# Performance work log

Measured on AMD Instinct MI355X. Metric: run time of the kernel, lower is better.

Reference implementation:

```python
import jax, jax.numpy as jnp
import numpy as np

B, K, LQ, LR, H = 32, 8, 128, 256, 512  # H = hidden_dim*2
L = LQ + K * LR


def setup_inputs() -> dict:
    key = jax.random.key(0)
    ks = jax.random.split(key, 10)
    w = 0.02
    return {
        "h_q": jax.random.normal(ks[0], (B, LQ, H), jnp.float32),
        "q_mask": jnp.ones((B, LQ), jnp.float32),
        "h_r": jax.random.normal(ks[1], (B, K, LR, H), jnp.float32),
        "r_mask": jnp.ones((B, K, LR), jnp.float32),
        "s_t": jax.random.normal(ks[2], (B, H), jnp.float32),
        "qr_cov": jnp.zeros((B, L), jnp.float32),
        # Linear weights stored torch-style [out, in]
        "U_w": jax.random.normal(ks[3], (H, H), jnp.float32) * w,
        "Wc_w": jax.random.normal(ks[4], (H, 1), jnp.float32) * w,
        "Ws_w": jax.random.normal(ks[5], (H, H), jnp.float32) * w,
        "Wqr_w": jax.random.normal(ks[6], (H, H), jnp.float32) * w,
        "Wqr_b": jax.random.normal(ks[7], (H,), jnp.float32) * w,
        "Vr_w": jax.random.normal(ks[8], (1, H), jnp.float32) * w,
    }


def reference(h_q, q_mask, h_r, r_mask, s_t, qr_cov,
              U_w, Wc_w, Ws_w, Wqr_w, Wqr_b, Vr_w):
    b, l_q, h = h_q.shape
    _, k, l_r, _ = h_r.shape

    _h_q = jnp.broadcast_to(h_q[:, None], (b, k, l_q, h)).reshape(b * k, l_q, h)
    _h_r = h_r.reshape(b * k, l_r, h)
    _q_mask = jnp.broadcast_to(q_mask[:, None], (b, k, l_q)).reshape(b * k, l_q)
    _r_mask = r_mask.reshape(b * k, l_r)

    # bilinear co-attention scores: tanh((hq @ U^T) @ hr^T)  [b*k, l_q, l_r]
    hqU = jnp.einsum('bqi,oi->bqo', _h_q, U_w)
    U = jnp.tanh(jnp.einsum('bqo,bro->bqr', hqU, _h_r))

    alpha_q = jax.nn.softmax(jnp.max(U, axis=2), axis=-1)  # [b*k, l_q]
    alpha_r = jax.nn.softmax(jnp.max(U, axis=1), axis=-1)  # [b*k, l_r]

    pai_q = ((alpha_q * _q_mask)[..., None] * _h_q).reshape(b, k, l_q, h).mean(axis=1)
    pai_r = ((alpha_r * _r_mask)[..., None] * _h_r).reshape(b, k * l_r, h)
    qr = jnp.concatenate([pai_q, pai_r], axis=1)  # [b, L, h]

    dec_fea = (jnp.einsum('bi,oi->bo', s_t, Ws_w)[:, None, :]
               + jnp.einsum('bli,oi->blo', qr, Wqr_w) + Wqr_b
               + qr_cov[:, :, None] * Wc_w[:, 0])  # coverage feature

    logits = jnp.einsum('blo,o->bl', jnp.tanh(dec_fea), Vr_w[0])  # [b, L]
    mask = jnp.concatenate([q_mask, r_mask.reshape(b, k * l_r)], axis=1)
    a = jax.nn.softmax(logits, axis=1) * mask
    a = a / jnp.sum(a, axis=1, keepdims=True)

    c_t = jnp.einsum('bl,blh->bh', a, qr)
    new_cov = qr_cov + a
    return (c_t, a, new_cov)
```

## Files before the change

kernel.cpp:

```cpp
#include <hip/hip_runtime.h>
#include <hip/hip_fp8.h>
#include <stdint.h>

#define B  32
#define KK 8
#define LQ 128
#define LR 256
#define H  512
#define LL 2176

typedef short s16x8 __attribute__((ext_vector_type(8)));
typedef float f32x4 __attribute__((ext_vector_type(4)));
typedef int   i32x8 __attribute__((ext_vector_type(8)));

__device__ __forceinline__ unsigned short f2bf(float f) {
    unsigned int u = __float_as_uint(f);
    unsigned int r = (u + 0x7FFFu + ((u >> 16) & 1u)) >> 16;
    return (unsigned short)r;
}
__device__ __forceinline__ unsigned char f2fp8(float f) {
    __hip_fp8_e4m3 v(f);
    return (unsigned char)v.__x;
}
__device__ __forceinline__ unsigned int pk_fp8(float a, float b) {
#if __has_builtin(__builtin_amdgcn_cvt_pk_fp8_f32)
    return (unsigned int)__builtin_amdgcn_cvt_pk_fp8_f32(a, b, 0, false) & 0xFFFFu;
#else
    return (unsigned int)f2fp8(a) | ((unsigned int)f2fp8(b) << 8);
#endif
}
__device__ __forceinline__ unsigned int pk_bf16(float a, float b) {
    return (unsigned int)f2bf(a) | ((unsigned int)f2bf(b) << 16);
}
__device__ __forceinline__ void gload16(const void* g, void* l) {
    __builtin_amdgcn_global_load_lds(
        (const __attribute__((address_space(1))) void*)g,
        (__attribute__((address_space(3))) void*)l, 16, 0, 0);
}
__device__ __forceinline__ float fexp2(float x) {
#if __has_builtin(__builtin_amdgcn_exp2f)
    return __builtin_amdgcn_exp2f(x);
#else
    return __expf(x * 0.69314718056f);
#endif
}
__device__ __forceinline__ float frcp(float x) {
#if __has_builtin(__builtin_amdgcn_rcpf)
    return __builtin_amdgcn_rcpf(x);
#else
    return 1.f / x;
#endif
}
__device__ __forceinline__ float fast_tanh(float x) {
    float e = fexp2(x * 2.885390082f);
    return 1.f - 2.f * frcp(1.f + e);
}
#define LOG2E 1.4426950408889634f

#define NQ4 (B * LQ * H / 4)
#define NR4 (B * KK * LR * H / 4)
#define NL4 (B * LL / 4)
#define NC4 (B * H / 4)
#define NWB4 (B * LL / 4)
#define SBLK 256
#define WBLK 64
#define ZBLK 19
#define QBLK 256
#define RBLK 4096
#define K0GRID (SBLK + WBLK + ZBLK + QBLK + RBLK)
__global__ __launch_bounds__(256) void k0_convert(
    const float* __restrict__ h_q, const float* __restrict__ h_r,
    const float* __restrict__ U_w, const float* __restrict__ Wqr_w,
    unsigned short* __restrict__ Xb, unsigned short* __restrict__ Uwb,
    unsigned char* __restrict__ Xb8, unsigned char* __restrict__ Wqrb8,
    float* __restrict__ logits, float* __restrict__ out_ct,
    float* __restrict__ wbuf, const float* __restrict__ s_t,
    const float* __restrict__ Ws_w, float* __restrict__ sWs) {
    int t = threadIdx.x;
    int blk = blockIdx.x;
    if (blk < SBLK) {
        int b = blk >> 3, oc = blk & 7;
        __shared__ __align__(16) float sl[H];
        for (int i = t; i < H; i += 256) sl[i] = s_t[b * H + i];
        __syncthreads();
        int o = oc * 64 + (t >> 2);
        int part = t & 3;
        const float4* sl4 = (const float4*)sl;
        const float4* wr4 = (const float4*)(Ws_w + (size_t)o * H);
        float a = 0.f;
#pragma unroll
        for (int ii = 0; ii < 32; ++ii) {
            int i = part + 4 * ii;
            float4 x = sl4[i], y = wr4[i];
            a += x.x * y.x + x.y * y.y + x.z * y.z + x.w * y.w;
        }
        a += __shfl_xor(a, 1);
        a += __shfl_xor(a, 2);
        if (part == 0) sWs[b * H + o] = a;
        return;
    }
    blk -= SBLK;
    if (blk < WBLK) {
        bool isU = (blk < 32);
        unsigned base = (unsigned)(blk & 31) * 2048u;
        const float4* src = isU ? (const float4*)U_w : (const float4*)Wqr_w;
        uint4* dst = isU ? (uint4*)Uwb : (uint4*)((unsigned short*)Xb + 0);
        uint4* dstW = (uint4*)((unsigned char*)0);
        (void)dstW;
#pragma unroll
        for (int jj = 0; jj < 4; ++jj) {
            unsigned f4i = base + (unsigned)jj * 512u + 2u * (unsigned)t;
            float4 v0 = src[f4i], v1 = src[f4i + 1];
            uint4 ob;
            ob.x = pk_bf16(v0.x, v0.y); ob.y = pk_bf16(v0.z, v0.w);
            ob.z = pk_bf16(v1.x, v1.y); ob.w = pk_bf16(v1.z, v1.w);
            if (isU) {
                ((uint4*)Uwb)[f4i >> 1] = ob;
            } else {
                uint2 o8;
                o8.x = pk_fp8(v0.x, v0.y) | (pk_fp8(v0.z, v0.w) << 16);
                o8.y = pk_fp8(v1.x, v1.y) | (pk_fp8(v1.z, v1.w) << 16);
                ((uint2*)Wqrb8)[f4i >> 1] = o8;
            }
        }
        return;
    }
    blk -= WBLK;
    if (blk < ZBLK) {
        unsigned zb = (unsigned)blk;
        float4 zero = {0.f, 0.f, 0.f, 0.f};
        float4* lg4 = (float4*)logits;
        float4* ct4 = (float4*)out_ct;
        float4* wb4 = (float4*)wbuf;
#pragma unroll
        for (int j = 0; j < 8; ++j) {
            unsigned z = zb * 2048u + (unsigned)j * 256u + (unsigned)t;
            if (z < NL4) lg4[z] = zero;
            else if (z < NL4 + NC4) ct4[z - NL4] = zero;
            else if (z < NL4 + NC4 + NWB4) wb4[z - NL4 - NC4] = zero;
        }
        return;
    }
    blk -= ZBLK;
    {
        const float4* src; unsigned dstoff;
        if (blk < QBLK) {
            unsigned u0 = (unsigned)blk * 2048u;
            unsigned b = (unsigned)blk >> 3;
            src = (const float4*)h_q + u0;
            dstoff = b * 278528u + (u0 & 16383u);
        } else {
            unsigned rb = (unsigned)(blk - QBLK);
            unsigned u0 = rb * 2048u;
            unsigned b = rb >> 7;
            src = (const float4*)h_r + u0;
            dstoff = b * 278528u + 16384u + (u0 & 262143u);
        }
        uint4* dstb = (uint4*)Xb;
        uint2* dst8 = (uint2*)Xb8;
#pragma unroll
        for (int jj = 0; jj < 4; ++jj) {
            unsigned loc = (unsigned)jj * 512u + 2u * (unsigned)t;
            float4 v0 = src[loc], v1 = src[loc + 1];
            unsigned idx = (dstoff + loc) >> 1;
            uint4 ob;
            ob.x = pk_bf16(v0.x, v0.y); ob.y = pk_bf16(v0.z, v0.w);
            ob.z = pk_bf16(v1.x, v1.y); ob.w = pk_bf16(v1.z, v1.w);
            dstb[idx] = ob;
            uint2 o8;
            o8.x = pk_fp8(v0.x, v0.y) | (pk_fp8(v0.z, v0.w) << 16);
            o8.y = pk_fp8(v1.x, v1.y) | (pk_fp8(v1.z, v1.w) << 16);
            dst8[idx] = o8;
        }
    }
}

__global__ __launch_bounds__(256) void k1_gemm_hqU(
    const unsigned short* __restrict__ Xb, const unsigned short* __restrict__ Uwb,
    unsigned char* __restrict__ hqU8) {
    __shared__ __align__(16) unsigned short As[64 * 64];
    __shared__ __align__(16) unsigned short Bs[128 * 64];
    int tid = threadIdx.x;
    int wave = tid >> 6, lane = tid & 63;
    int quad = lane >> 4, l16 = lane & 15;
    int wr = wave >> 1, wc = wave & 1;
    int g = blockIdx.x;
    int tle = (g & 7) * 32 + (g >> 3);
    int mt = tle >> 2, nt = tle & 3;
    int m0 = mt * 64, n0 = nt * 128;

    const unsigned short* ag[2]; unsigned short* la[2];
    const unsigned short* bg[4]; unsigned short* lb[4];
#pragma unroll
    for (int i = 0; i < 2; ++i) {
        int gg = (wave * 2 + i) * 64 + lane;
        int r = gg >> 3, c = gg & 7, cs = c ^ (r & 7);
        int am = m0 + r;
        ag[i] = Xb + ((size_t)(am >> 7) * LL + (am & 127)) * H + cs * 8;
        la[i] = As + (wave * 2 + i) * 512;
    }
#pragma unroll
    for (int i = 0; i < 4; ++i) {
        int gg = (wave * 4 + i) * 64 + lane;
        int r = gg >> 3, c = gg & 7, cs = c ^ (r & 7);
        bg[i] = Uwb + (size_t)(n0 + r) * H + cs * 8;
        lb[i] = Bs + (wave * 4 + i) * 512;
    }

    f32x4 acc[2][4] = {};
    for (int k0 = 0; k0 < H; k0 += 64) {
#pragma unroll
        for (int i = 0; i < 2; ++i) gload16(ag[i] + k0, la[i]);
#pragma unroll
        for (int i = 0; i < 4; ++i) gload16(bg[i] + k0, lb[i]);
        __syncthreads();
#pragma unroll
        for (int kh = 0; kh < 2; ++kh) {
            s16x8 af[2], bfr[4];
#pragma unroll
            for (int mi = 0; mi < 2; ++mi) {
                int row = wr * 32 + mi * 16 + l16;
                int ch = (kh * 4 + quad) ^ (row & 7);
                af[mi] = *(const s16x8*)&As[(row * 8 + ch) * 8];
            }
#pragma unroll
            for (int ni = 0; ni < 4; ++ni) {
                int row = wc * 64 + ni * 16 + l16;
                int ch = (kh * 4 + quad) ^ (row & 7);
                bfr[ni] = *(const s16x8*)&Bs[(row * 8 + ch) * 8];
            }
#pragma unroll
            for (int mi = 0; mi < 2; ++mi)
#pragma unroll
                for (int ni = 0; ni < 4; ++ni)
                    acc[mi][ni] = __builtin_amdgcn_mfma_f32_16x16x32_bf16(
                        af[mi], bfr[ni], acc[mi][ni], 0, 0, 0);
        }
        __syncthreads();
    }
#pragma unroll
    for (int mi = 0; mi < 2; ++mi)
#pragma unroll
        for (int ni = 0; ni < 4; ++ni)
#pragma unroll
            for (int i = 0; i < 4; ++i) {
                float v = acc[mi][ni][i];
                float vn = __shfl_xor(v, 1);
                if ((l16 & 1) == 0) {
                    int row = m0 + wr * 32 + mi * 16 + quad * 4 + i;
                    int col = n0 + wc * 64 + ni * 16 + l16;
                    unsigned short pk = (unsigned short)pk_fp8(v, vn);
                    *(unsigned short*)(hqU8 + (size_t)row * H + col) = pk;
                }
            }
}

__global__ __launch_bounds__(256) void k2_scores(
    const unsigned char* __restrict__ hqU8, const unsigned char* __restrict__ Xb8,
    float* __restrict__ maxq, float* __restrict__ maxr_part) {
    __shared__ __align__(16) unsigned char As[64 * 128];
    __shared__ __align__(16) unsigned char Bs[256 * 128];
    __shared__ float redA[64 * 2];
    __shared__ float redB[256 * 2];
    int g = blockIdx.x;
    int tle = (g & 7) * 64 + (g >> 3);
    int qt = tle & 1, k = (tle >> 1) & 7, b = tle >> 4;
    int tid = threadIdx.x;
    int wave = tid >> 6, lane = tid & 63;
    int quad = lane >> 4, l16 = lane & 15;
    int wr = wave >> 1, wc = wave & 1;

    const unsigned char* Ab = hqU8 + (size_t)(b * LQ + qt * 64) * H;
    const unsigned char* Bb = Xb8 + (size_t)(b * LL + LQ + k * LR) * H;

    const unsigned char* ag[2]; unsigned char* la[2];
    const unsigned char* bg[8]; unsigned char* lb[8];
#pragma unroll
    for (int i = 0; i < 2; ++i) {
        int gg = (wave * 2 + i) * 64 + lane;
        int r = gg >> 3, c = gg & 7, cs = c ^ (r & 7);
        ag[i] = Ab + (size_t)r * H + cs * 16;
        la[i] = As + gg * 16;
    }
#pragma unroll
    for (int i = 0; i < 8; ++i) {
        int gg = (wave * 8 + i) * 64 + lane;
        int r = gg >> 3, c = gg & 7, cs = c ^ (r & 7);
        bg[i] = Bb + (size_t)r * H + cs * 16;
        lb[i] = Bs + gg * 16;
    }

    f32x4 acc[2][8] = {};
    for (int k0 = 0; k0 < H; k0 += 128) {
#pragma unroll
        for (int i = 0; i < 2; ++i) gload16(ag[i] + k0, la[i]);
#pragma unroll
        for (int i = 0; i < 8; ++i) gload16(bg[i] + k0, lb[i]);
        __syncthreads();
        i32x8 af[2];
#pragma unroll
        for (int mi = 0; mi < 2; ++mi) {
            int row = wr * 32 + mi * 16 + l16;
            int xs = row & 7;
            const uint4* rp = (const uint4*)(As + row * 128);
            uint4 lo = rp[(quad * 2) ^ xs];
            uint4 hi = rp[(quad * 2 + 1) ^ xs];
            af[mi][0] = lo.x; af[mi][1] = lo.y; af[mi][2] = lo.z; af[mi][3] = lo.w;
            af[mi][4] = hi.x; af[mi][5] = hi.y; af[mi][6] = hi.z; af[mi][7] = hi.w;
        }
#pragma unroll
        for (int ni = 0; ni < 8; ++ni) {
            int row = wc * 128 + ni * 16 + l16;
            int xs = row & 7;
            const uint4* rp = (const uint4*)(Bs + row * 128);
            uint4 lo = rp[(quad * 2) ^ xs];
            uint4 hi = rp[(quad * 2 + 1) ^ xs];
            i32x8 bfr;
            bfr[0] = lo.x; bfr[1] = lo.y; bfr[2] = lo.z; bfr[3] = lo.w;
            bfr[4] = hi.x; bfr[5] = hi.y; bfr[6] = hi.z; bfr[7] = hi.w;
#pragma unroll
            for (int mi = 0; mi < 2; ++mi)
                acc[mi][ni] = __builtin_amdgcn_mfma_scale_f32_16x16x128_f8f6f4(
                    af[mi], bfr, acc[mi][ni], 0, 0,
                    0, 0x7F7F7F7F, 0, 0x7F7F7F7F);
        }
        __syncthreads();
    }
#pragma unroll
    for (int mi = 0; mi < 2; ++mi)
#pragma unroll
        for (int i = 0; i < 4; ++i) {
            float v = acc[mi][0][i];
#pragma unroll
            for (int ni = 1; ni < 8; ++ni) v = fmaxf(v, acc[mi][ni][i]);
            for (int s = 1; s < 16; s <<= 1) v = fmaxf(v, __shfl_xor(v, s));
            if (l16 == 0) redA[(wr * 32 + mi * 16 + quad * 4 + i) * 2 + wc] = v;
        }
#pragma unroll
    for (int ni = 0; ni < 8; ++ni) {
        float v = acc[0][ni][0];
#pragma unroll
        for (int mi = 0; mi < 2; ++mi)
#pragma unroll
            for (int i = 0; i < 4; ++i) v = fmaxf(v, acc[mi][ni][i]);
        for (int s = 16; s < 64; s <<= 1) v = fmaxf(v, __shfl_xor(v, s));
        if (quad == 0) redB[(wc * 128 + ni * 16 + l16) * 2 + wr] = v;
    }
    __syncthreads();
    size_t bk = (size_t)(b * KK + k);
    if (tid < 64)
        maxq[bk * 128 + qt * 64 + tid] = fmaxf(redA[tid * 2 + 0], redA[tid * 2 + 1]);
    maxr_part[(bk * 2 + qt) * 256 + tid] = fmaxf(redB[tid * 2 + 0], redB[tid * 2 + 1]);
}

__global__ __launch_bounds__(256) void k3_alphas(
    const float* __restrict__ maxq, const float* __restrict__ maxr_part,
    const float* __restrict__ r_mask, const float* __restrict__ q_mask,
    float* __restrict__ wbuf) {
    int b = blockIdx.x >> 3, k = blockIdx.x & 7;
    int t = threadIdx.x;
    __shared__ float red[256];
    size_t bk = (size_t)(b * KK + k);
    float vq = -1e30f;
    if (t < 128) vq = fast_tanh(maxq[bk * 128 + t]);
    red[t] = vq; __syncthreads();
    for (int s = 128; s > 0; s >>= 1) { if (t < s) red[t] = fmaxf(red[t], red[t + s]); __syncthreads(); }
    float mxq = red[0]; __syncthreads();
    float eq = (t < 128) ? fexp2((vq - mxq) * LOG2E) : 0.f;
    red[t] = eq; __syncthreads();
    for (int s = 128; s > 0; s >>= 1) { if (t < s) red[t] += red[t + s]; __syncthreads(); }
    float invq = 1.f / red[0]; __syncthreads();
    if (t < 128)
        atomicAdd(&wbuf[b * LL + t], q_mask[b * LQ + t] * eq * invq * 0.125f);
    float vr = fast_tanh(fmaxf(maxr_part[(bk * 2 + 0) * 256 + t],
                               maxr_part[(bk * 2 + 1) * 256 + t]));
    red[t] = vr; __syncthreads();
    for (int s = 128; s > 0; s >>= 1) { if (t < s) red[t] = fmaxf(red[t], red[t + s]); __syncthreads(); }
    float mxr = red[0]; __syncthreads();
    float er = fexp2((vr - mxr) * LOG2E);
    red[t] = er; __syncthreads();
    for (int s = 128; s > 0; s >>= 1) { if (t < s) red[t] += red[t + s]; __syncthreads(); }
    float invr = 1.f / red[0];
    wbuf[b * LL + LQ + k * LR + t] = r_mask[bk * LR + t] * er * invr;
}

__global__ __launch_bounds__(256) void k4_gemm_logits(
    const unsigned char* __restrict__ Xb8, const unsigned char* __restrict__ Wqrb8,
    const float* __restrict__ sWs, const float* __restrict__ Wqr_b,
    const float* __restrict__ Wc_w, const float* __restrict__ Vr_w,
    const float* __restrict__ wbuf, const float* __restrict__ qr_cov,
    float* __restrict__ logits) {
    __shared__ __align__(16) unsigned char As[128 * 128];
    __shared__ __align__(16) unsigned char Bs[128 * 128];
    __shared__ float wrow[128], covrow[128], sWsl[128], biasl[128], wcl[128], vrl[128];
    int tid = threadIdx.x;
    int wave = tid >> 6, lane = tid & 63;
    int quad = lane >> 4, l16 = lane & 15;
    int wr = wave >> 1, wc = wave & 1;
    int g = blockIdx.x;
    int tle = (g & 7) * 272 + (g >> 3);
    int mt = tle >> 2, nt = tle & 3;
    size_t m0 = (size_t)mt * 128;
    int n0 = nt * 128;
    int b = mt / 17;

    if (tid < 128) {
        wrow[tid]   = wbuf[m0 + tid];
        covrow[tid] = qr_cov[m0 + tid];
        sWsl[tid]   = sWs[b * H + n0 + tid];
        biasl[tid]  = Wqr_b[n0 + tid];
        wcl[tid]    = Wc_w[n0 + tid];
        vrl[tid]    = Vr_w[n0 + tid];
    }

    const unsigned char* ag[4]; unsigned char* la[4];
    const unsigned char* bg[4]; unsigned char* lb[4];
#pragma unroll
    for (int i = 0; i < 4; ++i) {
        int gg = (wave * 4 + i) * 64 + lane;
        int r = gg >> 3, c = gg & 7, cs = c ^ (r & 7);
        ag[i] = Xb8 + (m0 + r) * H + cs * 16;
        bg[i] = Wqrb8 + (size_t)(n0 + r) * H + cs * 16;
        la[i] = As + (wave * 4 + i) * 1024;
        lb[i] = Bs + (wave * 4 + i) * 1024;
    }

    f32x4 acc[4][4] = {};
    for (int k0 = 0; k0 < H; k0 += 128) {
#pragma unroll
        for (int i = 0; i < 4; ++i) gload16(ag[i] + k0, la[i]);
#pragma unroll
        for (int i = 0; i < 4; ++i) gload16(bg[i] + k0, lb[i]);
        __syncthreads();
        i32x8 af[4];
#pragma unroll
        for (int mi = 0; mi < 4; ++mi) {
            int row = wr * 64 + mi * 16 + l16;
            int xs = row & 7;
            const uint4* rp = (const uint4*)(As + row * 128);
            uint4 lo = rp[(quad * 2) ^ xs];
            uint4 hi = rp[(quad * 2 + 1) ^ xs];
            af[mi][0] = lo.x; af[mi][1] = lo.y; af[mi][2] = lo.z; af[mi][3] = lo.w;
            af[mi][4] = hi.x; af[mi][5] = hi.y; af[mi][6] = hi.z; af[mi][7] = hi.w;
        }
#pragma unroll
        for (int ni = 0; ni < 4; ++ni) {
            int row = wc * 64 + ni * 16 + l16;
            int xs = row & 7;
            const uint4* rp = (const uint4*)(Bs + row * 128);
            uint4 lo = rp[(quad * 2) ^ xs];
            uint4 hi = rp[(quad * 2 + 1) ^ xs];
            i32x8 bfr;
            bfr[0] = lo.x; bfr[1] = lo.y; bfr[2] = lo.z; bfr[3] = lo.w;
            bfr[4] = hi.x; bfr[5] = hi.y; bfr[6] = hi.z; bfr[7] = hi.w;
#pragma unroll
            for (int mi = 0; mi < 4; ++mi)
                acc[mi][ni] = __builtin_amdgcn_mfma_scale_f32_16x16x128_f8f6f4(
                    af[mi], bfr, acc[mi][ni], 0, 0,
                    0, 0x7F7F7F7F, 0, 0x7F7F7F7F);
        }
        __syncthreads();
    }
#pragma unroll
    for (int mi = 0; mi < 4; ++mi)
#pragma unroll
        for (int i = 0; i < 4; ++i) {
            int rl = wr * 64 + mi * 16 + quad * 4 + i;
            float wv = wrow[rl], cv = covrow[rl];
            float lsum = 0.f;
#pragma unroll
            for (int ni = 0; ni < 4; ++ni) {
                int ol = wc * 64 + ni * 16 + l16;
                float dec = sWsl[ol] + wv * acc[mi][ni][i] + biasl[ol] + cv * wcl[ol];
                lsum += vrl[ol] * fast_tanh(dec);
            }
            for (int s = 1; s < 16; s <<= 1) lsum += __shfl_xor(lsum, s);
            if (l16 == 0) atomicAdd(&logits[m0 + rl], lsum);
        }
}

__global__ __launch_bounds__(256) void k5a_softmax(
    const float* __restrict__ logits, const float* __restrict__ q_mask,
    const float* __restrict__ r_mask, const float* __restrict__ qr_cov,
    const float* __restrict__ wbuf, float* __restrict__ out,
    float* __restrict__ coef) {
    int b = blockIdx.x, t = threadIdx.x;
    __shared__ float lg[LL];
    __shared__ float red[256];
    float mx = -1e30f;
    for (int l = t; l < LL; l += 256) {
        float v = logits[b * LL + l];
        lg[l] = v;
        mx = fmaxf(mx, v);
    }
    red[t] = mx; __syncthreads();
    for (int s = 128; s > 0; s >>= 1) { if (t < s) red[t] = fmaxf(red[t], red[t + s]); __syncthreads(); }
    mx = red[0]; __syncthreads();
    float sum = 0.f;
    for (int l = t; l < LL; l += 256) {
        float e = fexp2((lg[l] - mx) * LOG2E);
        float m = (l < LQ) ? q_mask[b * LQ + l] : r_mask[b * (KK * LR) + l - LQ];
        float em = e * m;
        lg[l] = em;
        sum += em;
    }
    red[t] = sum; __syncthreads();
    for (int s = 128; s > 0; s >>= 1) { if (t < s) red[t] += red[t + s]; __syncthreads(); }
    float inv = 1.f / red[0];
    __syncthreads();
    float* aout = out + B * H + (size_t)b * LL;
    float* cov  = out + B * H + (size_t)B * LL + (size_t)b * LL;
    for (int l = t; l < LL; l += 256) {
        float a = lg[l] * inv;
        aout[l] = a;
        cov[l] = qr_cov[b * LL + l] + a;
        coef[b * LL + l] = a * wbuf[b * LL + l];
    }
}

__global__ __launch_bounds__(256) void k5b_ct(
    const unsigned short* __restrict__ Xb, const float* __restrict__ coef,
    float* __restrict__ out) {
    int b = blockIdx.x / 34, chunk = blockIdx.x % 34;
    int t = threadIdx.x;
    int l0 = chunk * 64;
    __shared__ float cl[64];
    __shared__ float red[4][512];
    if (t < 64) cl[t] = coef[b * LL + l0 + t];
    __syncthreads();
    int rr = t >> 6, lane = t & 63, cc = lane * 8;
    float a[8] = {};
    const unsigned short* xp = Xb + ((size_t)b * LL + l0) * H;
    for (int l = rr; l < 64; l += 4) {
        float c = cl[l];
        uint4 u4 = *(const uint4*)(xp + (size_t)l * H + cc);
        a[0] += c * __uint_as_float(u4.x << 16);
        a[1] += c * __uint_as_float(u4.x & 0xffff0000u);
        a[2] += c * __uint_as_float(u4.y << 16);
        a[3] += c * __uint_as_float(u4.y & 0xffff0000u);
        a[4] += c * __uint_as_float(u4.z << 16);
        a[5] += c * __uint_as_float(u4.z & 0xffff0000u);
        a[6] += c * __uint_as_float(u4.w << 16);
        a[7] += c * __uint_as_float(u4.w & 0xffff0000u);
    }
#pragma unroll
    for (int j = 0; j < 8; ++j) red[rr][cc + j] = a[j];
    __syncthreads();
    int col = t * 2;
    float s0 = red[0][col] + red[1][col] + red[2][col] + red[3][col];
    float s1 = red[0][col + 1] + red[1][col + 1] + red[2][col + 1] + red[3][col + 1];
    atomicAdd(&out[b * H + col], s0);
    atomicAdd(&out[b * H + col + 1], s1);
}

extern "C" void kernel_launch(void* const* d_in, const int* in_sizes, int n_in,
                              void* d_out, int out_size, void* d_ws, size_t ws_size,
                              hipStream_t stream) {
    (void)in_sizes; (void)n_in; (void)out_size; (void)ws_size;
    const float* h_q    = (const float*)d_in[0];
    const float* q_mask = (const float*)d_in[1];
    const float* h_r    = (const float*)d_in[2];
    const float* r_mask = (const float*)d_in[3];
    const float* s_t    = (const float*)d_in[4];
    const float* qr_cov = (const float*)d_in[5];
    const float* U_w    = (const float*)d_in[6];
    const float* Wc_w   = (const float*)d_in[7];
    const float* Ws_w   = (const float*)d_in[8];
    const float* Wqr_w  = (const float*)d_in[9];
    const float* Wqr_b  = (const float*)d_in[10];
    const float* Vr_w   = (const float*)d_in[11];
    float* out = (float*)d_out;

    char* p = (char*)d_ws;
    unsigned short* Xb    = (unsigned short*)p; p += (size_t)B * LL * H * 2;
    unsigned char*  Xb8   = (unsigned char*)p;  p += (size_t)B * LL * H;
    unsigned short* Uwb   = (unsigned short*)p; p += (size_t)H * H * 2;
    unsigned char*  Wqrb8 = (unsigned char*)p;  p += (size_t)H * H;
    unsigned char*  hqU8  = (unsigned char*)p;  p += (size_t)B * LQ * H;
    float* sWs       = (float*)p; p += (size_t)B * H * 4;
    float* maxq      = (float*)p; p += (size_t)B * KK * 128 * 4;
    float* maxr_part = (float*)p; p += (size_t)B * KK * 2 * 256 * 4;
    float* wbuf      = (float*)p; p += (size_t)B * LL * 4;
    float* logits    = (float*)p; p += (size_t)B * LL * 4;
    float* coef      = (float*)p; p += (size_t)B * LL * 4;

    k0_convert<<<K0GRID, 256, 0, stream>>>(h_q, h_r, U_w, Wqr_w, Xb, Uwb,
                                           Xb8, Wqrb8, logits, out, wbuf,
                                           s_t, Ws_w, sWs);
    k1_gemm_hqU<<<256, 256, 0, stream>>>(Xb, Uwb, hqU8);
    k2_scores<<<512, 256, 0, stream>>>(hqU8, Xb8, maxq, maxr_part);
    k3_alphas<<<B * KK, 256, 0, stream>>>(maxq, maxr_part, r_mask, q_mask, wbuf);
    k4_gemm_logits<<<2176, 256, 0, stream>>>(
        Xb8, Wqrb8, sWs, Wqr_b, Wc_w, Vr_w, wbuf, qr_cov, logits);
    k5a_softmax<<<B, 256, 0, stream>>>(logits, q_mask, r_mask, qr_cov, wbuf, out, coef);
    k5b_ct<<<B * 34, 256, 0, stream>>>(Xb, coef, out);
}
```

Before: 361.2 us.

## Drop full bf16 activation copy, read fp32 inputs in context kernel, shrink logits tiles

```diff
diff --git a/kernel.cpp b/kernel.cpp
--- a/kernel.cpp
+++ b/kernel.cpp
@@ -22,11 +22,14 @@
     __hip_fp8_e4m3 v(f);
     return (unsigned char)v.__x;
 }
-__device__ __forceinline__ unsigned int pk_fp8(float a, float b) {
+__device__ __forceinline__ unsigned int pk_fp8x4(float a, float b, float c, float d) {
 #if __has_builtin(__builtin_amdgcn_cvt_pk_fp8_f32)
-    return (unsigned int)__builtin_amdgcn_cvt_pk_fp8_f32(a, b, 0, false) & 0xFFFFu;
+    int w = __builtin_amdgcn_cvt_pk_fp8_f32(a, b, 0, false);
+    w = __builtin_amdgcn_cvt_pk_fp8_f32(c, d, w, true);
+    return (unsigned int)w;
 #else
-    return (unsigned int)f2fp8(a) | ((unsigned int)f2fp8(b) << 8);
+    return (unsigned int)f2fp8(a) | ((unsigned int)f2fp8(b) << 8) |
+           ((unsigned int)f2fp8(c) << 16) | ((unsigned int)f2fp8(d) << 24);
 #endif
 }
 __device__ __forceinline__ unsigned int pk_bf16(float a, float b) {
@@ -57,8 +60,6 @@
 }
 #define LOG2E 1.4426950408889634f
 
-#define NQ4 (B * LQ * H / 4)
-#define NR4 (B * KK * LR * H / 4)
 #define NL4 (B * LL / 4)
 #define NC4 (B * H / 4)
 #define NWB4 (B * LL / 4)
@@ -71,7 +72,7 @@
 __global__ __launch_bounds__(256) void k0_convert(
     const float* __restrict__ h_q, const float* __restrict__ h_r,
     const float* __restrict__ U_w, const float* __restrict__ Wqr_w,
-    unsigned short* __restrict__ Xb, unsigned short* __restrict__ Uwb,
+    unsigned short* __restrict__ Xq, unsigned short* __restrict__ Uwb,
     unsigned char* __restrict__ Xb8, unsigned char* __restrict__ Wqrb8,
     float* __restrict__ logits, float* __restrict__ out_ct,
     float* __restrict__ wbuf, const float* __restrict__ s_t,
@@ -104,22 +105,19 @@
         bool isU = (blk < 32);
         unsigned base = (unsigned)(blk & 31) * 2048u;
         const float4* src = isU ? (const float4*)U_w : (const float4*)Wqr_w;
-        uint4* dst = isU ? (uint4*)Uwb : (uint4*)((unsigned short*)Xb + 0);
-        uint4* dstW = (uint4*)((unsigned char*)0);
-        (void)dstW;
 #pragma unroll
         for (int jj = 0; jj < 4; ++jj) {
             unsigned f4i = base + (unsigned)jj * 512u + 2u * (unsigned)t;
             float4 v0 = src[f4i], v1 = src[f4i + 1];
-            uint4 ob;
-            ob.x = pk_bf16(v0.x, v0.y); ob.y = pk_bf16(v0.z, v0.w);
-            ob.z = pk_bf16(v1.x, v1.y); ob.w = pk_bf16(v1.z, v1.w);
             if (isU) {
+                uint4 ob;
+                ob.x = pk_bf16(v0.x, v0.y); ob.y = pk_bf16(v0.z, v0.w);
+                ob.z = pk_bf16(v1.x, v1.y); ob.w = pk_bf16(v1.z, v1.w);
                 ((uint4*)Uwb)[f4i >> 1] = ob;
             } else {
                 uint2 o8;
-                o8.x = pk_fp8(v0.x, v0.y) | (pk_fp8(v0.z, v0.w) << 16);
-                o8.y = pk_fp8(v1.x, v1.y) | (pk_fp8(v1.z, v1.w) << 16);
+                o8.x = pk_fp8x4(v0.x, v0.y, v0.z, v0.w);
+                o8.y = pk_fp8x4(v1.x, v1.y, v1.z, v1.w);
                 ((uint2*)Wqrb8)[f4i >> 1] = o8;
             }
         }
@@ -142,41 +140,46 @@
         return;
     }
     blk -= ZBLK;
-    {
-        const float4* src; unsigned dstoff;
-        if (blk < QBLK) {
-            unsigned u0 = (unsigned)blk * 2048u;
-            unsigned b = (unsigned)blk >> 3;
-            src = (const float4*)h_q + u0;
-            dstoff = b * 278528u + (u0 & 16383u);
-        } else {
-            unsigned rb = (unsigned)(blk - QBLK);
-            unsigned u0 = rb * 2048u;
-            unsigned b = rb >> 7;
-            src = (const float4*)h_r + u0;
-            dstoff = b * 278528u + 16384u + (u0 & 262143u);
-        }
-        uint4* dstb = (uint4*)Xb;
-        uint2* dst8 = (uint2*)Xb8;
+    if (blk < QBLK) {
+        unsigned u0 = (unsigned)blk * 2048u;
+        unsigned b = (unsigned)blk >> 3;
+        const float4* src = (const float4*)h_q + u0;
 #pragma unroll
         for (int jj = 0; jj < 4; ++jj) {
             unsigned loc = (unsigned)jj * 512u + 2u * (unsigned)t;
             float4 v0 = src[loc], v1 = src[loc + 1];
-            unsigned idx = (dstoff + loc) >> 1;
             uint4 ob;
             ob.x = pk_bf16(v0.x, v0.y); ob.y = pk_bf16(v0.z, v0.w);
             ob.z = pk_bf16(v1.x, v1.y); ob.w = pk_bf16(v1.z, v1.w);
-            dstb[idx] = ob;
+            ((uint4*)Xq)[(u0 + loc) >> 1] = ob;
             uint2 o8;
-            o8.x = pk_fp8(v0.x, v0.y) | (pk_fp8(v0.z, v0.w) << 16);
-            o8.y = pk_fp8(v1.x, v1.y) | (pk_fp8(v1.z, v1.w) << 16);
-            dst8[idx] = o8;
+            o8.x = pk_fp8x4(v0.x, v0.y, v0.z, v0.w);
+            o8.y = pk_fp8x4(v1.x, v1.y, v1.z, v1.w);
+            unsigned f8off = b * 278528u + ((u0 + loc) & 16383u);
+            ((uint2*)Xb8)[f8off >> 1] = o8;
+        }
+        return;
+    }
+    {
+        unsigned rb = (unsigned)(blk - QBLK);
+        unsigned u0 = rb * 2048u;
+        unsigned b = rb >> 7;
+        const float4* src = (const float4*)h_r + u0;
+#pragma unroll
+        for (int jj = 0; jj < 4; ++jj) {
+            unsigned loc = (unsigned)jj * 512u + 2u * (unsigned)t;
+            float4 v0 = src[loc], v1 = src[loc + 1];
+            uint2 o8;
+            o8.x = pk_fp8x4(v0.x, v0.y, v0.z, v0.w);
+            o8.y = pk_fp8x4(v1.x, v1.y, v1.z, v1.w);
+            unsigned f8off = b * 278528u + 16384u + ((u0 + loc) & 262143u);
+            ((uint2*)Xb8)[f8off >> 1] = o8;
         }
     }
 }
 
 __global__ __launch_bounds__(256) void k1_gemm_hqU(
-    const unsigned short* __restrict__ Xb, const unsigned short* __restrict__ Uwb,
+    const unsigned short* __restrict__ Xq, const unsigned short* __restrict__ Uwb,
     unsigned char* __restrict__ hqU8) {
     __shared__ __align__(16) unsigned short As[64 * 64];
     __shared__ __align__(16) unsigned short Bs[128 * 64];
@@ -195,8 +198,7 @@
     for (int i = 0; i < 2; ++i) {
         int gg = (wave * 2 + i) * 64 + lane;
         int r = gg >> 3, c = gg & 7, cs = c ^ (r & 7);
-        int am = m0 + r;
-        ag[i] = Xb + ((size_t)(am >> 7) * LL + (am & 127)) * H + cs * 8;
+        ag[i] = Xq + (size_t)(m0 + r) * H + cs * 8;
         la[i] = As + (wave * 2 + i) * 512;
     }
 #pragma unroll
@@ -249,7 +251,8 @@
                 if ((l16 & 1) == 0) {
                     int row = m0 + wr * 32 + mi * 16 + quad * 4 + i;
                     int col = n0 + wc * 64 + ni * 16 + l16;
-                    unsigned short pk = (unsigned short)pk_fp8(v, vn);
+                    unsigned short pk = (unsigned short)
+                        (pk_fp8x4(v, vn, 0.f, 0.f) & 0xFFFFu);
                     *(unsigned short*)(hqU8 + (size_t)row * H + col) = pk;
                 }
             }
@@ -384,27 +387,27 @@
     wbuf[b * LL + LQ + k * LR + t] = r_mask[bk * LR + t] * er * invr;
 }
 
-__global__ __launch_bounds__(256) void k4_gemm_logits(
+__global__ __launch_bounds__(256, 4) void k4_gemm_logits(
     const unsigned char* __restrict__ Xb8, const unsigned char* __restrict__ Wqrb8,
     const float* __restrict__ sWs, const float* __restrict__ Wqr_b,
     const float* __restrict__ Wc_w, const float* __restrict__ Vr_w,
     const float* __restrict__ wbuf, const float* __restrict__ qr_cov,
     float* __restrict__ logits) {
-    __shared__ __align__(16) unsigned char As[128 * 128];
-    __shared__ __align__(16) unsigned char Bs[128 * 128];
-    __shared__ float wrow[128], covrow[128], sWsl[128], biasl[128], wcl[128], vrl[128];
+    __shared__ __align__(16) unsigned char As[64 * 128];
+    __shared__ __align__(16) unsigned char Bs[64 * 128];
+    __shared__ float wrow[64], covrow[64], sWsl[64], biasl[64], wcl[64], vrl[64];
     int tid = threadIdx.x;
     int wave = tid >> 6, lane = tid & 63;
     int quad = lane >> 4, l16 = lane & 15;
     int wr = wave >> 1, wc = wave & 1;
     int g = blockIdx.x;
-    int tle = (g & 7) * 272 + (g >> 3);
-    int mt = tle >> 2, nt = tle & 3;
-    size_t m0 = (size_t)mt * 128;
-    int n0 = nt * 128;
-    int b = mt / 17;
-
-    if (tid < 128) {
+    int tle = (g & 7) * 1088 + (g >> 3);
+    int mt = tle >> 3, nt = tle & 7;
+    size_t m0 = (size_t)mt * 64;
+    int n0 = nt * 64;
+    int b = mt / 34;
+
+    if (tid < 64) {
         wrow[tid]   = wbuf[m0 + tid];
         covrow[tid] = qr_cov[m0 + tid];
         sWsl[tid]   = sWs[b * H + n0 + tid];
@@ -413,29 +416,29 @@
         vrl[tid]    = Vr_w[n0 + tid];
     }
 
-    const unsigned char* ag[4]; unsigned char* la[4];
-    const unsigned char* bg[4]; unsigned char* lb[4];
-#pragma unroll
-    for (int i = 0; i < 4; ++i) {
-        int gg = (wave * 4 + i) * 64 + lane;
+    const unsigned char* ag[2]; unsigned char* la[2];
+    const unsigned char* bg[2]; unsigned char* lb[2];
+#pragma unroll
+    for (int i = 0; i < 2; ++i) {
+        int gg = (wave * 2 + i) * 64 + lane;
         int r = gg >> 3, c = gg & 7, cs = c ^ (r & 7);
         ag[i] = Xb8 + (m0 + r) * H + cs * 16;
         bg[i] = Wqrb8 + (size_t)(n0 + r) * H + cs * 16;
-        la[i] = As + (wave * 4 + i) * 1024;
-        lb[i] = Bs + (wave * 4 + i) * 1024;
-    }
-
-    f32x4 acc[4][4] = {};
+        la[i] = As + gg * 16;
+        lb[i] = Bs + gg * 16;
+    }
+
+    f32x4 acc[2][2] = {};
     for (int k0 = 0; k0 < H; k0 += 128) {
 #pragma unroll
-        for (int i = 0; i < 4; ++i) gload16(ag[i] + k0, la[i]);
-#pragma unroll
-        for (int i = 0; i < 4; ++i) gload16(bg[i] + k0, lb[i]);
-        __syncthreads();
-        i32x8 af[4];
-#pragma unroll
-        for (int mi = 0; mi < 4; ++mi) {
-            int row = wr * 64 + mi * 16 + l16;
+        for (int i = 0; i < 2; ++i) gload16(ag[i] + k0, la[i]);
+#pragma unroll
+        for (int i = 0; i < 2; ++i) gload16(bg[i] + k0, lb[i]);
+        __syncthreads();
+        i32x8 af[2];
+#pragma unroll
+        for (int mi = 0; mi < 2; ++mi) {
+            int row = wr * 32 + mi * 16 + l16;
             int xs = row & 7;
             const uint4* rp = (const uint4*)(As + row * 128);
             uint4 lo = rp[(quad * 2) ^ xs];
@@ -444,8 +447,8 @@
             af[mi][4] = hi.x; af[mi][5] = hi.y; af[mi][6] = hi.z; af[mi][7] = hi.w;
         }
 #pragma unroll
-        for (int ni = 0; ni < 4; ++ni) {
-            int row = wc * 64 + ni * 16 + l16;
+        for (int ni = 0; ni < 2; ++ni) {
+            int row = wc * 32 + ni * 16 + l16;
             int xs = row & 7;
             const uint4* rp = (const uint4*)(Bs + row * 128);
             uint4 lo = rp[(quad * 2) ^ xs];
@@ -454,7 +457,7 @@
             bfr[0] = lo.x; bfr[1] = lo.y; bfr[2] = lo.z; bfr[3] = lo.w;
             bfr[4] = hi.x; bfr[5] = hi.y; bfr[6] = hi.z; bfr[7] = hi.w;
 #pragma unroll
-            for (int mi = 0; mi < 4; ++mi)
+            for (int mi = 0; mi < 2; ++mi)
                 acc[mi][ni] = __builtin_amdgcn_mfma_scale_f32_16x16x128_f8f6f4(
                     af[mi], bfr, acc[mi][ni], 0, 0,
                     0, 0x7F7F7F7F, 0, 0x7F7F7F7F);
@@ -462,15 +465,15 @@
         __syncthreads();
     }
 #pragma unroll
-    for (int mi = 0; mi < 4; ++mi)
+    for (int mi = 0; mi < 2; ++mi)
 #pragma unroll
         for (int i = 0; i < 4; ++i) {
-            int rl = wr * 64 + mi * 16 + quad * 4 + i;
+            int rl = wr * 32 + mi * 16 + quad * 4 + i;
             float wv = wrow[rl], cv = covrow[rl];
             float lsum = 0.f;
 #pragma unroll
-            for (int ni = 0; ni < 4; ++ni) {
-                int ol = wc * 64 + ni * 16 + l16;
+            for (int ni = 0; ni < 2; ++ni) {
+                int ol = wc * 32 + ni * 16 + l16;
                 float dec = sWsl[ol] + wv * acc[mi][ni][i] + biasl[ol] + cv * wcl[ol];
                 lsum += vrl[ol] * fast_tanh(dec);
             }
@@ -519,8 +522,8 @@
 }
 
 __global__ __launch_bounds__(256) void k5b_ct(
-    const unsigned short* __restrict__ Xb, const float* __restrict__ coef,
-    float* __restrict__ out) {
+    const float* __restrict__ h_q, const float* __restrict__ h_r,
+    const float* __restrict__ coef, float* __restrict__ out) {
     int b = blockIdx.x / 34, chunk = blockIdx.x % 34;
     int t = threadIdx.x;
     int l0 = chunk * 64;
@@ -528,20 +531,17 @@
     __shared__ float red[4][512];
     if (t < 64) cl[t] = coef[b * LL + l0 + t];
     __syncthreads();
+    const float* src = (chunk < 2)
+        ? h_q + ((size_t)b * LQ + l0) * H
+        : h_r + ((size_t)b * (KK * LR) + (l0 - LQ)) * H;
     int rr = t >> 6, lane = t & 63, cc = lane * 8;
     float a[8] = {};
-    const unsigned short* xp = Xb + ((size_t)b * LL + l0) * H;
     for (int l = rr; l < 64; l += 4) {
         float c = cl[l];
-        uint4 u4 = *(const uint4*)(xp + (size_t)l * H + cc);
-        a[0] += c * __uint_as_float(u4.x << 16);
-        a[1] += c * __uint_as_float(u4.x & 0xffff0000u);
-        a[2] += c * __uint_as_float(u4.y << 16);
-        a[3] += c * __uint_as_float(u4.y & 0xffff0000u);
-        a[4] += c * __uint_as_float(u4.z << 16);
-        a[5] += c * __uint_as_float(u4.z & 0xffff0000u);
-        a[6] += c * __uint_as_float(u4.w << 16);
-        a[7] += c * __uint_as_float(u4.w & 0xffff0000u);
+        float4 x0 = *(const float4*)(src + (size_t)l * H + cc);
+        float4 x1 = *(const float4*)(src + (size_t)l * H + cc + 4);
+        a[0] += c * x0.x; a[1] += c * x0.y; a[2] += c * x0.z; a[3] += c * x0.w;
+        a[4] += c * x1.x; a[5] += c * x1.y; a[6] += c * x1.z; a[7] += c * x1.w;
     }
 #pragma unroll
     for (int j = 0; j < 8; ++j) red[rr][cc + j] = a[j];
@@ -572,8 +572,8 @@
     float* out = (float*)d_out;
 
     char* p = (char*)d_ws;
-    unsigned short* Xb    = (unsigned short*)p; p += (size_t)B * LL * H * 2;
     unsigned char*  Xb8   = (unsigned char*)p;  p += (size_t)B * LL * H;
+    unsigned short* Xq    = (unsigned short*)p; p += (size_t)B * LQ * H * 2;
     unsigned short* Uwb   = (unsigned short*)p; p += (size_t)H * H * 2;
     unsigned char*  Wqrb8 = (unsigned char*)p;  p += (size_t)H * H;
     unsigned char*  hqU8  = (unsigned char*)p;  p += (size_t)B * LQ * H;
@@ -584,14 +584,14 @@
     float* logits    = (float*)p; p += (size_t)B * LL * 4;
     float* coef      = (float*)p; p += (size_t)B * LL * 4;
 
-    k0_convert<<<K0GRID, 256, 0, stream>>>(h_q, h_r, U_w, Wqr_w, Xb, Uwb,
+    k0_convert<<<K0GRID, 256, 0, stream>>>(h_q, h_r, U_w, Wqr_w, Xq, Uwb,
                                            Xb8, Wqrb8, logits, out, wbuf,
                                            s_t, Ws_w, sWs);
-    k1_gemm_hqU<<<256, 256, 0, stream>>>(Xb, Uwb, hqU8);
+    k1_gemm_hqU<<<256, 256, 0, stream>>>(Xq, Uwb, hqU8);
     k2_scores<<<512, 256, 0, stream>>>(hqU8, Xb8, maxq, maxr_part);
     k3_alphas<<<B * KK, 256, 0, stream>>>(maxq, maxr_part, r_mask, q_mask, wbuf);
-    k4_gemm_logits<<<2176, 256, 0, stream>>>(
+    k4_gemm_logits<<<8704, 256, 0, stream>>>(
         Xb8, Wqrb8, sWs, Wqr_b, Wc_w, Vr_w, wbuf, qr_cov, logits);
     k5a_softmax<<<B, 256, 0, stream>>>(logits, q_mask, r_mask, qr_cov, wbuf, out, coef);
-    k5b_ct<<<B * 34, 256, 0, stream>>>(Xb, coef, out);
-}
+    k5b_ct<<<B * 34, 256, 0, stream>>>(h_q, h_r, coef, out);
+}
```

Result: faster. 344.0 us (-4.8%).
